# Optimization experiments

Measured on AMD Instinct MI355X. Metric: run time of the kernel, lower is better.

Reference implementation:

```python
import jax, jax.numpy as jnp
import numpy as np

NUM_ROUTE_NODES = 1152
IN_CHANNELS = 8
OUT_CHANNELS = 16
NUM_DIGITS = 10
NUM_ITERATIONS = 3
BATCH = 256


def squash(x):
    # Faithful to the original: uses the GLOBAL norm of the whole tensor,
    # not a per-capsule norm.
    norm = jnp.linalg.norm(x)
    sq = norm * norm
    return (sq / (1.0 + sq)) * (x / norm)


def setup_inputs() -> dict:
    key = jax.random.key(0)
    k_u, k_w = jax.random.split(key)
    u = jax.random.normal(k_u, (BATCH, NUM_ROUTE_NODES, IN_CHANNELS), dtype=jnp.float32)
    # W: (1, R, D, out, in) as in nn.Parameter(torch.randn(...))
    W = jax.random.normal(k_w, (1, NUM_ROUTE_NODES, NUM_DIGITS, OUT_CHANNELS, IN_CHANNELS), dtype=jnp.float32)
    return {"u": u, "W": W}


def reference(u, W):
    # u_hat[b,r,d,o] = sum_i W[0,r,d,o,i] * u[b,r,i]
    u_hat = jnp.einsum('rdoi,bri->brdo', W[0], u)  # (B, R, D, O)
    R, D = u_hat.shape[1], u_hat.shape[2]
    b = jnp.zeros((R, D), dtype=u_hat.dtype)
    v = None
    for _ in range(NUM_ITERATIONS):
        c = jax.nn.softmax(b, axis=1)[None, :, :, None]     # (1, R, D, 1)
        s = jnp.sum(u_hat * c, axis=1)                      # (B, D, O)
        v = squash(s)                                       # (B, D, O)
        # agreement: a[b,r,d] = sum_o u_hat[b,r,d,o] * v[b,d,o]
        a = jnp.einsum('brdo,bdo->brd', u_hat, v)           # (B, R, D)
        b = b + jnp.sum(a, axis=0)                          # (R, D)
    return v
```

## Files before the change

kernel.cpp:

```cpp
#include <hip/hip_runtime.h>
#include <math.h>

#define R_NODES 1152
#define DIGITS 10
#define OUT_CH 16
#define IN_CH 8
#define BATCH 256
#define COLS 160
#define W_PER_R 1280
#define MROW 9216
#define NSPLIT 72
#define RPS 16
#define YB_S 4
#define UP 88
#define KB 72
#define BLOG_N 11520

typedef __attribute__((ext_vector_type(8))) short short8v;
typedef __attribute__((ext_vector_type(4))) float floatx4;

__device__ inline unsigned short f2bf(float x) {
    union { float f; unsigned int i; } v; v.f = x;
    unsigned int r = v.i + 0x7FFFu + ((v.i >> 16) & 1u);
    return (unsigned short)(r >> 16);
}
__device__ inline float bf2f(unsigned short x) {
    union { unsigned int i; float f; } v; v.i = ((unsigned int)x) << 16;
    return v.f;
}

__global__ __launch_bounds__(512, 2) void k_s(
    const float* __restrict__ u,
    const float* __restrict__ W,
    const float* __restrict__ blog4,
    unsigned short* __restrict__ part,
    float* __restrict__ sqz,
    int nbuf)
{
    __shared__ unsigned short ulds[64 * UP];
    __shared__ unsigned short wlds[COLS * UP];
    __shared__ float cs[RPS * DIGITS];

    const int split = blockIdx.x;
    const int b0 = blockIdx.y * 64;
    const int t = threadIdx.x;
    const int r0 = split * RPS;

    if (split == 0 && blockIdx.y == 0 && t == 0) *sqz = 0.f;

    if (t < RPS * DIGITS) {
        float a = 0.f;
        if (nbuf) {
            a = blog4[r0 * DIGITS + t]
              + blog4[BLOG_N + r0 * DIGITS + t]
              + blog4[2 * BLOG_N + r0 * DIGITS + t]
              + blog4[3 * BLOG_N + r0 * DIGITS + t];
        }
        cs[t] = a;
    }
    __syncthreads();
    if (t < RPS) {
        float e[DIGITS];
        float m = -1e30f;
#pragma unroll
        for (int d = 0; d < DIGITS; ++d) m = fmaxf(m, cs[t*10 + d]);
        float ssum = 0.f;
#pragma unroll
        for (int d = 0; d < DIGITS; ++d) { e[d] = expf(cs[t*10 + d] - m); ssum += e[d]; }
        float inv = 1.f / ssum;
#pragma unroll
        for (int d = 0; d < DIGITS; ++d) cs[t*10 + d] = e[d] * inv;
    }
    __syncthreads();

    const int w = t >> 6, l = t & 63;
    const int mtile = w & 3;
    const int ncol0 = (w >> 2) * 5;
    const int koff = (l >> 4) * 8;
    const int arow = (mtile * 16 + (l & 15)) * UP;

    floatx4 acc[5];
#pragma unroll
    for (int j = 0; j < 5; ++j) acc[j] = (floatx4){0.f, 0.f, 0.f, 0.f};

    for (int ch = 0; ch < 2; ++ch) {
        const int rc = r0 + ch * 8;
        float4 uv[2];
#pragma unroll
        for (int p = 0; p < 2; ++p) {
            int idx = t + p * 512;
            int b = idx >> 4, q = idx & 15;
            uv[p] = *(const float4*)(u + (size_t)(b0 + b) * (R_NODES * IN_CH)
                                       + (size_t)rc * IN_CH + q * 4);
        }
        float4 wr[5];
        {
            const float4* Wg = (const float4*)(W + (size_t)rc * W_PER_R);
#pragma unroll
            for (int p = 0; p < 5; ++p) wr[p] = Wg[t + p * 512];
        }
        if (ch) __syncthreads();
#pragma unroll
        for (int p = 0; p < 2; ++p) {
            int idx = t + p * 512;
            int b = idx >> 4, q = idx & 15;
            *(short4*)&ulds[b * UP + q * 4] =
                make_short4((short)f2bf(uv[p].x), (short)f2bf(uv[p].y),
                            (short)f2bf(uv[p].z), (short)f2bf(uv[p].w));
        }
#pragma unroll
        for (int p = 0; p < 5; ++p) {
            int e4 = t + p * 512;
            int e  = e4 * 4;
            int r_l = e4 / 320;
            int rem = e - r_l * W_PER_R;
            int col = rem >> 3;
            int i0  = e & 7;
            float cv = cs[(ch * 8 + r_l) * 10 + (rem >> 7)];
            float4 w4 = wr[p];
            *(short4*)&wlds[col * UP + r_l * 8 + i0] =
                make_short4((short)f2bf(w4.x * cv), (short)f2bf(w4.y * cv),
                            (short)f2bf(w4.z * cv), (short)f2bf(w4.w * cv));
        }
        __syncthreads();
        short8v a0 = *(const short8v*)&ulds[arow + koff];
        short8v a1 = *(const short8v*)&ulds[arow + 32 + koff];
#pragma unroll
        for (int j = 0; j < 5; ++j) {
            const int bcol = ((ncol0 + j) * 16 + (l & 15)) * UP;
            short8v bb0 = *(const short8v*)&wlds[bcol + koff];
            short8v bb1 = *(const short8v*)&wlds[bcol + 32 + koff];
            acc[j] = __builtin_amdgcn_mfma_f32_16x16x32_bf16(a0, bb0, acc[j], 0, 0, 0);
            acc[j] = __builtin_amdgcn_mfma_f32_16x16x32_bf16(a1, bb1, acc[j], 0, 0, 0);
        }
    }

    unsigned short* pp = part + (size_t)split * (BATCH * COLS);
    const int gb = b0 + mtile * 16 + (l >> 4) * 4;
#pragma unroll
    for (int j = 0; j < 5; ++j) {
        const int gc = (ncol0 + j) * 16 + (l & 15);
#pragma unroll
        for (int reg = 0; reg < 4; ++reg)
            pp[(size_t)(gb + reg) * COLS + gc] = f2bf(acc[j][reg]);
    }
}

__global__ void k_sq(const unsigned short* __restrict__ part,
                     float* __restrict__ s,
                     float* __restrict__ sq)
{
    const int t = threadIdx.x;
    const int e0 = blockIdx.x * 64;
    const int el = t & 63, q = t >> 6;
    float v = 0.f;
    for (int sp = q; sp < NSPLIT; sp += 4)
        v += bf2f(part[(size_t)sp * (BATCH * COLS) + e0 + el]);
    __shared__ float red[256];
    red[t] = v;
    __syncthreads();
    if (t < 64) {
        float vv = red[t] + red[t + 64] + red[t + 128] + red[t + 192];
        s[e0 + t] = vv;
        float x = vv * vv;
#pragma unroll
        for (int off = 32; off > 0; off >>= 1)
            x += __shfl_down(x, off, 64);
        if (t == 0) atomicAdd(sq, x);
    }
}

__global__ __launch_bounds__(256, 3) void k_b(
    const float* __restrict__ u,
    const float* __restrict__ s,
    const float* __restrict__ W,
    const float* __restrict__ sqp,
    float* __restrict__ blog4,
    int first)
{
    __shared__ unsigned short uld[64 * KB];
    __shared__ unsigned short sld[16 * KB];
    const int t = threadIdx.x;
    const int rig = blockIdx.x;
    const int bq = blockIdx.y;
    const int b0 = bq * 64;

#pragma unroll
    for (int p = 0; p < 4; ++p) {
        int idx = t + p * 256;
        int b = idx >> 4, q = idx & 15;
        float4 v = *(const float4*)(u + (size_t)(b0 + b) * MROW + rig * 64 + q * 4);
        uld[(q*4+0)*KB + b] = f2bf(v.x);
        uld[(q*4+1)*KB + b] = f2bf(v.y);
        uld[(q*4+2)*KB + b] = f2bf(v.z);
        uld[(q*4+3)*KB + b] = f2bf(v.w);
    }

    const int w = t >> 6, l = t & 63;
    const float q0 = *sqp;
    const float scale = sqrtf(q0) / (1.f + q0);
    const int r_l = 2 * w + ((l & 15) >> 3);
    const int r = rig * 8 + r_l;
    float* slot = blog4 + (size_t)bq * BLOG_N;

    for (int d = 0; d < DIGITS; ++d) {
        int sb = t >> 2, sq_ = t & 3;
        float4 v = *(const float4*)(s + (size_t)(b0 + sb) * COLS + d * 16 + sq_ * 4);
        if (d) __syncthreads();
        sld[(sq_*4+0)*KB + sb] = f2bf(v.x);
        sld[(sq_*4+1)*KB + sb] = f2bf(v.y);
        sld[(sq_*4+2)*KB + sb] = f2bf(v.z);
        sld[(sq_*4+3)*KB + sb] = f2bf(v.w);
        __syncthreads();

        floatx4 acc = {0.f, 0.f, 0.f, 0.f};
#pragma unroll
        for (int ks = 0; ks < 2; ++ks) {
            int koff = ks * 32 + (l >> 4) * 8;
            short8v av = *(const short8v*)&sld[(l & 15) * KB + koff];
            short8v bv = *(const short8v*)&uld[(w * 16 + (l & 15)) * KB + koff];
            acc = __builtin_amdgcn_mfma_f32_16x16x32_bf16(av, bv, acc, 0, 0, 0);
        }

        const float* Wp = W + (size_t)r * W_PER_R + d * 128 + (l & 7);
        float p = 0.f;
#pragma unroll
        for (int reg = 0; reg < 4; ++reg) {
            int o = (l >> 4) * 4 + reg;
            p = fmaf(Wp[o * 8], acc[reg], p);
        }
        p += __shfl_xor(p, 1, 64);
        p += __shfl_xor(p, 2, 64);
        p += __shfl_xor(p, 4, 64);
        p += __shfl_xor(p, 16, 64);
        p += __shfl_xor(p, 32, 64);

        if ((l & 55) == 0) {
            float prev = first ? 0.f : slot[r * DIGITS + d];
            slot[r * DIGITS + d] = prev + scale * p;
        }
    }
}

__global__ void k_scale(const float* __restrict__ s,
                        const float* __restrict__ sq,
                        float* __restrict__ out)
{
    int e = blockIdx.x * 256 + threadIdx.x;
    float q = *sq;
    float scale = sqrtf(q) / (1.f + q);
    out[e] = s[e] * scale;
}

extern "C" void kernel_launch(void* const* d_in, const int* in_sizes, int n_in,
                              void* d_out, int out_size, void* d_ws, size_t ws_size,
                              hipStream_t stream)
{
    const float* u = (const float*)d_in[0];
    const float* W = (const float*)d_in[1];
    float* out = (float*)d_out;
    float* ws = (float*)d_ws;

    float* s     = ws;
    float* sqbuf = ws + 40960;
    float* blog4 = ws + 41024;
    unsigned short* part = (unsigned short*)(ws + 41024 + 4 * BLOG_N + 64);

    for (int it = 0; it < 3; ++it) {
        k_s<<<dim3(NSPLIT, YB_S), dim3(512), 0, stream>>>(u, W, blog4, part,
                                                          sqbuf + it, it);
        k_sq<<<dim3(BATCH * COLS / 64), dim3(256), 0, stream>>>(part, s, sqbuf + it);
        if (it < 2)
            k_b<<<dim3(144, 4), dim3(256), 0, stream>>>(u, s, W, sqbuf + it,
                                                        blog4, it == 0 ? 1 : 0);
        else
            k_scale<<<dim3(BATCH * COLS / 256), dim3(256), 0, stream>>>(s, sqbuf + 2, out);
    }
}
```

Measured before the change: 96.05 us.

## Fuse split reduction into agreement and final-scale kernels with atomic counter sync

Merges the partial-sum reduction kernel into the agreement kernel: the first 160 blocks reduce the bf16 partials and bump a global counter, while the remaining blocks stage u into LDS and then spin on the counter before reading the squared-norm. The final iteration fuses reduction and scaling into one kernel with an in-kernel grid barrier. This removes two kernel launches per call and overlaps u staging with the reduction. It relies on all reducer blocks being scheduled before waiters could deadlock, and adds spin-wait and atomic contention.

After: 138.6 us. 44.3% more time.

```diff
diff --git a/kernel.cpp b/kernel.cpp
--- a/kernel.cpp
+++ b/kernel.cpp
@@ -15,6 +15,7 @@
 #define UP 88
 #define KB 72
 #define BLOG_N 11520
+#define NSQB 160
 
 typedef __attribute__((ext_vector_type(8))) short short8v;
 typedef __attribute__((ext_vector_type(4))) float floatx4;
@@ -35,6 +36,7 @@
     const float* __restrict__ blog4,
     unsigned short* __restrict__ part,
     float* __restrict__ sqz,
+    int* __restrict__ ctrz,
     int nbuf)
 {
     __shared__ unsigned short ulds[64 * UP];
@@ -46,7 +48,7 @@
     const int t = threadIdx.x;
     const int r0 = split * RPS;
 
-    if (split == 0 && blockIdx.y == 0 && t == 0) *sqz = 0.f;
+    if (split == 0 && blockIdx.y == 0 && t == 0) { *sqz = 0.f; *ctrz = 0; }
 
     if (t < RPS * DIGITS) {
         float a = 0.f;
@@ -146,49 +148,56 @@
     }
 }
 
-__global__ void k_sq(const unsigned short* __restrict__ part,
-                     float* __restrict__ s,
-                     float* __restrict__ sq)
-{
-    const int t = threadIdx.x;
-    const int e0 = blockIdx.x * 64;
-    const int el = t & 63, q = t >> 6;
-    float v = 0.f;
-    for (int sp = q; sp < NSPLIT; sp += 4)
-        v += bf2f(part[(size_t)sp * (BATCH * COLS) + e0 + el]);
-    __shared__ float red[256];
-    red[t] = v;
-    __syncthreads();
-    if (t < 64) {
-        float vv = red[t] + red[t + 64] + red[t + 128] + red[t + 192];
-        s[e0 + t] = vv;
-        float x = vv * vv;
-#pragma unroll
-        for (int off = 32; off > 0; off >>= 1)
-            x += __shfl_down(x, off, 64);
-        if (t == 0) atomicAdd(sq, x);
-    }
-}
-
-__global__ __launch_bounds__(256, 3) void k_b(
+__global__ __launch_bounds__(256, 4) void k_qb(
+    const unsigned short* __restrict__ part,
+    float* __restrict__ s,
+    float* __restrict__ sq,
+    int* __restrict__ ctr,
     const float* __restrict__ u,
-    const float* __restrict__ s,
     const float* __restrict__ W,
-    const float* __restrict__ sqp,
     float* __restrict__ blog4,
     int first)
 {
+    const int t = threadIdx.x;
+
+    if (blockIdx.x < NSQB) {
+        __shared__ float red[256];
+        const int e = blockIdx.x * 256 + t;
+        float v = 0.f;
+#pragma unroll 8
+        for (int sp = 0; sp < NSPLIT; ++sp)
+            v += bf2f(part[(size_t)sp * (BATCH * COLS) + e]);
+        s[e] = v;
+        red[t] = v * v;
+        __syncthreads();
+        if (t < 128) red[t] += red[t + 128];
+        __syncthreads();
+        if (t < 64) {
+            float x = red[t] + red[t + 64];
+#pragma unroll
+            for (int off = 32; off > 0; off >>= 1)
+                x += __shfl_down(x, off, 64);
+            if (t == 0) atomicAdd(sq, x);
+        }
+        __syncthreads();
+        __threadfence();
+        if (t == 0)
+            __hip_atomic_fetch_add(ctr, 1, __ATOMIC_RELEASE, __HIP_MEMORY_SCOPE_AGENT);
+        return;
+    }
+
     __shared__ unsigned short uld[64 * KB];
     __shared__ unsigned short sld[16 * KB];
-    const int t = threadIdx.x;
-    const int rig = blockIdx.x;
-    const int bq = blockIdx.y;
+    __shared__ float scale_sh;
+    const int idx = blockIdx.x - NSQB;
+    const int rig = idx >> 2;
+    const int bq = idx & 3;
     const int b0 = bq * 64;
 
 #pragma unroll
     for (int p = 0; p < 4; ++p) {
-        int idx = t + p * 256;
-        int b = idx >> 4, q = idx & 15;
+        int i2 = t + p * 256;
+        int b = i2 >> 4, q = i2 & 15;
         float4 v = *(const float4*)(u + (size_t)(b0 + b) * MROW + rig * 64 + q * 4);
         uld[(q*4+0)*KB + b] = f2bf(v.x);
         uld[(q*4+1)*KB + b] = f2bf(v.y);
@@ -196,9 +205,16 @@
         uld[(q*4+3)*KB + b] = f2bf(v.w);
     }
 
+    if (t == 0) {
+        while (__hip_atomic_load(ctr, __ATOMIC_RELAXED, __HIP_MEMORY_SCOPE_AGENT) < NSQB) {}
+        (void)__hip_atomic_load(ctr, __ATOMIC_ACQUIRE, __HIP_MEMORY_SCOPE_AGENT);
+        float q0 = __hip_atomic_load(sq, __ATOMIC_RELAXED, __HIP_MEMORY_SCOPE_AGENT);
+        scale_sh = sqrtf(q0) / (1.f + q0);
+    }
+    __syncthreads();
+    const float scale = scale_sh;
+
     const int w = t >> 6, l = t & 63;
-    const float q0 = *sqp;
-    const float scale = sqrtf(q0) / (1.f + q0);
     const int r_l = 2 * w + ((l & 15) >> 3);
     const int r = rig * 8 + r_l;
     float* slot = blog4 + (size_t)bq * BLOG_N;
@@ -242,14 +258,41 @@
     }
 }
 
-__global__ void k_scale(const float* __restrict__ s,
-                        const float* __restrict__ sq,
-                        float* __restrict__ out)
+__global__ __launch_bounds__(256, 4) void k_qf(
+    const unsigned short* __restrict__ part,
+    float* __restrict__ sq,
+    int* __restrict__ ctr,
+    float* __restrict__ out)
 {
-    int e = blockIdx.x * 256 + threadIdx.x;
-    float q = *sq;
-    float scale = sqrtf(q) / (1.f + q);
-    out[e] = s[e] * scale;
+    const int t = threadIdx.x;
+    __shared__ float red[256];
+    __shared__ float scale_sh;
+    const int e = blockIdx.x * 256 + t;
+    float v = 0.f;
+#pragma unroll 8
+    for (int sp = 0; sp < NSPLIT; ++sp)
+        v += bf2f(part[(size_t)sp * (BATCH * COLS) + e]);
+    red[t] = v * v;
+    __syncthreads();
+    if (t < 128) red[t] += red[t + 128];
+    __syncthreads();
+    if (t < 64) {
+        float x = red[t] + red[t + 64];
+#pragma unroll
+        for (int off = 32; off > 0; off >>= 1)
+            x += __shfl_down(x, off, 64);
+        if (t == 0) atomicAdd(sq, x);
+    }
+    __syncthreads();
+    if (t == 0) {
+        __hip_atomic_fetch_add(ctr, 1, __ATOMIC_RELEASE, __HIP_MEMORY_SCOPE_AGENT);
+        while (__hip_atomic_load(ctr, __ATOMIC_RELAXED, __HIP_MEMORY_SCOPE_AGENT) < NSQB) {}
+        (void)__hip_atomic_load(ctr, __ATOMIC_ACQUIRE, __HIP_MEMORY_SCOPE_AGENT);
+        float q0 = __hip_atomic_load(sq, __ATOMIC_RELAXED, __HIP_MEMORY_SCOPE_AGENT);
+        scale_sh = sqrtf(q0) / (1.f + q0);
+    }
+    __syncthreads();
+    out[e] = v * scale_sh;
 }
 
 extern "C" void kernel_launch(void* const* d_in, const int* in_sizes, int n_in,
@@ -263,17 +306,18 @@
 
     float* s     = ws;
     float* sqbuf = ws + 40960;
+    int*   ctr   = (int*)(ws + 40992);
     float* blog4 = ws + 41024;
     unsigned short* part = (unsigned short*)(ws + 41024 + 4 * BLOG_N + 64);
 
     for (int it = 0; it < 3; ++it) {
         k_s<<<dim3(NSPLIT, YB_S), dim3(512), 0, stream>>>(u, W, blog4, part,
-                                                          sqbuf + it, it);
-        k_sq<<<dim3(BATCH * COLS / 64), dim3(256), 0, stream>>>(part, s, sqbuf + it);
+                                                          sqbuf + it, ctr + it, it);
         if (it < 2)
-            k_b<<<dim3(144, 4), dim3(256), 0, stream>>>(u, s, W, sqbuf + it,
-                                                        blog4, it == 0 ? 1 : 0);
+            k_qb<<<dim3(NSQB + 576), dim3(256), 0, stream>>>(part, s, sqbuf + it,
+                                                             ctr + it, u, W, blog4,
+                                                             it == 0 ? 1 : 0);
         else
-            k_scale<<<dim3(BATCH * COLS / 256), dim3(256), 0, stream>>>(s, sqbuf + 2, out);
-    }
-}
+            k_qf<<<dim3(NSQB), dim3(256), 0, stream>>>(part, sqbuf + 2, ctr + 2, out);
+    }
+}
```
